# Performance work log

Hardware: AMD Instinct MI355X
Metric: run time of the kernel (lower is better)

## Reference

```python
import jax, jax.numpy as jnp
import numpy as np

D_IN = 768
D_H = 256
N_CTX = 4

def setup_inputs() -> dict:
    key = jax.random.key(0)
    ks = jax.random.split(key, 6)
    b, s = 64, 2048
    return {
        "last_hidden_states": jax.random.normal(ks[0], (b, s, D_IN), dtype=jnp.float32),
        "W1": jax.random.normal(ks[1], (D_IN, D_H), dtype=jnp.float32) / np.sqrt(D_IN),
        "b1": jnp.zeros((D_H,), dtype=jnp.float32),
        "context_vector": jax.random.normal(ks[2], (D_H, N_CTX), dtype=jnp.float32),
        "W2": jax.random.normal(ks[3], (N_CTX * D_IN, D_IN), dtype=jnp.float32) / np.sqrt(N_CTX * D_IN),
        "b2": jnp.zeros((D_IN,), dtype=jnp.float32),
    }

def reference(last_hidden_states, W1, b1, context_vector, W2, b2):
    b = last_hidden_states.shape[0]
    # h: [b, s, 256]
    h = jnp.tanh(jnp.einsum('bsd,dh->bsh', last_hidden_states, W1) + b1)
    # scores over sequence dim for each of 4 context vectors: [b, s, 4]
    scores = jax.nn.softmax(jnp.einsum('bsh,hc->bsc', h, context_vector), axis=1)
    # weighted sums: [b, 4, 768] -> flatten to [b, 3072]
    pooled = jnp.einsum('bsc,bsd->bcd', scores, last_hidden_states).reshape(b, -1)
    pooled = jax.nn.relu(pooled)
    return pooled @ W2 + b2
```

## Files before the change

kernel.cpp:

```cpp
#include <hip/hip_runtime.h>

typedef _Float16 f16x8 __attribute__((ext_vector_type(8)));
typedef _Float16 f16x4 __attribute__((ext_vector_type(4)));
typedef float f32x4 __attribute__((ext_vector_type(4)));

#define D_IN 768
#define D_H  256
#define SEQ  2048

__device__ __forceinline__ void gld16(const void* g, void* l) {
  __builtin_amdgcn_global_load_lds(
      (const __attribute__((address_space(1))) unsigned int*)g,
      (__attribute__((address_space(3))) unsigned int*)l, 16, 0, 0);
}

__global__ __launch_bounds__(256) void k0_w1t(const float* __restrict__ W1,
                                              _Float16* __restrict__ W1T) {
  __shared__ float tl[64][65];
  const int kb = blockIdx.x, nb = blockIdx.y, t = threadIdx.x;
#pragma unroll
  for (int rep = 0; rep < 16; ++rep) {
    const int row = rep * 4 + (t >> 6), col = t & 63;
    tl[row][col] = W1[(size_t)(kb * 64 + row) * D_H + nb * 64 + col];
  }
  __syncthreads();
#pragma unroll
  for (int rep = 0; rep < 16; ++rep) {
    const int n = rep * 4 + (t >> 6), k = t & 63;
    W1T[(size_t)(nb * 64 + n) * D_IN + kb * 64 + k] = (_Float16)tl[k][n];
  }
}

__global__ __launch_bounds__(256, 4) void kf_fused(const float* __restrict__ X,
    const _Float16* __restrict__ W1T, const float* __restrict__ b1,
    const float* __restrict__ C, _Float16* __restrict__ Ppart,
    float* __restrict__ stats) {
  __shared__ float    Al[64][32];
  __shared__ _Float16 Bl[256][32];
  __shared__ float    red2[2][64][4];
  __shared__ float    red[64][4];
  const int t = threadIdx.x;
  const int bid = blockIdx.x;
  const size_t M0 = (size_t)bid * 64;

  const int l = t & 63, w = t >> 6;
  const int ar0 = (w * 2 + 0) * 8 + (l >> 3);
  const int ar1 = (w * 2 + 1) * 8 + (l >> 3);
  const int aj = l & 7;
  const float* As0 = X + (M0 + ar0) * D_IN + ((aj ^ (ar0 & 7)) * 4);
  const float* As1 = X + (M0 + ar1) * D_IN + ((aj ^ (ar1 & 7)) * 4);
  char* Ad0 = (char*)Al + (w * 2 + 0) * 1024 + l * 16;
  char* Ad1 = (char*)Al + (w * 2 + 1) * 1024 + l * 16;
  const int bj = l & 3;
  const int bc0 = (w * 4 + 0) * 16 + (l >> 2);
  const int bc1 = (w * 4 + 1) * 16 + (l >> 2);
  const int bc2 = (w * 4 + 2) * 16 + (l >> 2);
  const int bc3 = (w * 4 + 3) * 16 + (l >> 2);
  const _Float16* Bs0 = W1T + (size_t)bc0 * D_IN + ((bj ^ (bc0 & 3)) * 8);
  const _Float16* Bs1 = W1T + (size_t)bc1 * D_IN + ((bj ^ (bc1 & 3)) * 8);
  const _Float16* Bs2 = W1T + (size_t)bc2 * D_IN + ((bj ^ (bc2 & 3)) * 8);
  const _Float16* Bs3 = W1T + (size_t)bc3 * D_IN + ((bj ^ (bc3 & 3)) * 8);
  char* Bd0 = (char*)Bl + (w * 4 + 0) * 1024 + l * 16;
  char* Bd1 = (char*)Bl + (w * 4 + 1) * 1024 + l * 16;
  char* Bd2 = (char*)Bl + (w * 4 + 2) * 1024 + l * 16;
  char* Bd3 = (char*)Bl + (w * 4 + 3) * 1024 + l * 16;

  const int wm = w >> 1, wn = w & 1;
  const int l15 = l & 15, kg = l >> 4;
  const int r0 = wm * 32 + l15, r1 = r0 + 16;
  const int sA0lo = ((2 * kg) ^ (r0 & 7)) * 4, sA0hi = ((2 * kg + 1) ^ (r0 & 7)) * 4;
  const int sA1lo = ((2 * kg) ^ (r1 & 7)) * 4, sA1hi = ((2 * kg + 1) ^ (r1 & 7)) * 4;

  f32x4 acc[2][8];
#pragma unroll
  for (int i = 0; i < 2; ++i)
#pragma unroll
    for (int n = 0; n < 8; ++n) acc[i][n] = f32x4{0.f, 0.f, 0.f, 0.f};

  for (int kt = 0; kt < 24; ++kt) {
    const int ko = kt * 32;
    gld16(As0 + ko, Ad0);
    gld16(As1 + ko, Ad1);
    gld16(Bs0 + ko, Bd0);
    gld16(Bs1 + ko, Bd1);
    gld16(Bs2 + ko, Bd2);
    gld16(Bs3 + ko, Bd3);
    __syncthreads();

    const float4 a0lo = *(const float4*)&Al[r0][sA0lo];
    const float4 a0hi = *(const float4*)&Al[r0][sA0hi];
    const float4 a1lo = *(const float4*)&Al[r1][sA1lo];
    const float4 a1hi = *(const float4*)&Al[r1][sA1hi];
    f16x8 af0, af1;
    af0[0] = (_Float16)a0lo.x; af0[1] = (_Float16)a0lo.y;
    af0[2] = (_Float16)a0lo.z; af0[3] = (_Float16)a0lo.w;
    af0[4] = (_Float16)a0hi.x; af0[5] = (_Float16)a0hi.y;
    af0[6] = (_Float16)a0hi.z; af0[7] = (_Float16)a0hi.w;
    af1[0] = (_Float16)a1lo.x; af1[1] = (_Float16)a1lo.y;
    af1[2] = (_Float16)a1lo.z; af1[3] = (_Float16)a1lo.w;
    af1[4] = (_Float16)a1hi.x; af1[5] = (_Float16)a1hi.y;
    af1[6] = (_Float16)a1hi.z; af1[7] = (_Float16)a1hi.w;
#pragma unroll
    for (int n = 0; n < 8; ++n) {
      const int col = wn * 128 + n * 16 + l15;
      const f16x8 bf = *(const f16x8*)&Bl[col][(kg ^ (col & 3)) * 8];
      acc[0][n] = __builtin_amdgcn_mfma_f32_16x16x32_f16(af0, bf, acc[0][n], 0, 0, 0);
      acc[1][n] = __builtin_amdgcn_mfma_f32_16x16x32_f16(af1, bf, acc[1][n], 0, 0, 0);
    }
    __syncthreads();
  }

  float part[2][4][4];
#pragma unroll
  for (int i = 0; i < 2; ++i)
#pragma unroll
    for (int r = 0; r < 4; ++r)
#pragma unroll
      for (int c = 0; c < 4; ++c) part[i][r][c] = 0.f;

#pragma unroll
  for (int n = 0; n < 8; ++n) {
    const int col = wn * 128 + n * 16 + l15;
    const float4 c4 = *(const float4*)(C + col * 4);
    const float bv = b1[col];
#pragma unroll
    for (int i = 0; i < 2; ++i)
#pragma unroll
      for (int r = 0; r < 4; ++r) {
        float z = acc[i][n][r] + bv;
        z = fminf(fmaxf(z, -15.f), 15.f);
        const float e = __expf(2.f * z);
        const float h = (e - 1.f) / (e + 1.f);
        part[i][r][0] += h * c4.x;
        part[i][r][1] += h * c4.y;
        part[i][r][2] += h * c4.z;
        part[i][r][3] += h * c4.w;
      }
  }
#pragma unroll
  for (int off = 1; off < 16; off <<= 1) {
#pragma unroll
    for (int i = 0; i < 2; ++i)
#pragma unroll
      for (int r = 0; r < 4; ++r)
#pragma unroll
        for (int c = 0; c < 4; ++c)
          part[i][r][c] += __shfl_xor(part[i][r][c], off, 64);
  }
  if (l15 == 0) {
#pragma unroll
    for (int i = 0; i < 2; ++i)
#pragma unroll
      for (int r = 0; r < 4; ++r)
#pragma unroll
        for (int c = 0; c < 4; ++c)
          red2[wn][wm * 32 + i * 16 + kg * 4 + r][c] = part[i][r][c];
  }
  __syncthreads();

  {
    const int r = t >> 2, c = t & 3;
    red[r][c] = red2[0][r][c] + red2[1][r][c];
  }
  __syncthreads();
  {
    const int c = t >> 6, r = t & 63;
    const float v = red[r][c];
    float m = v;
#pragma unroll
    for (int off = 1; off < 64; off <<= 1) m = fmaxf(m, __shfl_xor(m, off, 64));
    const float e = __expf(v - m);
    red[r][c] = e;
    float s = e;
#pragma unroll
    for (int off = 1; off < 64; off <<= 1) s += __shfl_xor(s, off, 64);
    if (r == 0) {
      stats[(size_t)bid * 8 + c * 2]     = m;
      stats[(size_t)bid * 8 + c * 2 + 1] = s;
    }
  }
  __syncthreads();

  if (t < 192) {
    float pacc[4][4];
#pragma unroll
    for (int c = 0; c < 4; ++c)
#pragma unroll
      for (int j = 0; j < 4; ++j) pacc[c][j] = 0.f;
    const float* Xp = X + M0 * D_IN + t * 4;
#pragma unroll 4
    for (int r = 0; r < 64; ++r) {
      const float4 x4 = *(const float4*)(Xp + (size_t)r * D_IN);
      const float4 w4 = *(const float4*)&red[r][0];
      const float wc[4] = {w4.x, w4.y, w4.z, w4.w};
      const float xv[4] = {x4.x, x4.y, x4.z, x4.w};
#pragma unroll
      for (int c = 0; c < 4; ++c)
#pragma unroll
        for (int j = 0; j < 4; ++j) pacc[c][j] += wc[c] * xv[j];
    }
#pragma unroll
    for (int c = 0; c < 4; ++c) {
      f16x4 o;
#pragma unroll
      for (int j = 0; j < 4; ++j) o[j] = (_Float16)pacc[c][j];
      *(f16x4*)&Ppart[(size_t)bid * 3072 + c * 768 + t * 4] = o;
    }
  }
}

__global__ __launch_bounds__(256) void kc_combine(const _Float16* __restrict__ Ppart,
    const float* __restrict__ stats, float* __restrict__ pooled) {
  const int b = blockIdx.x, t = threadIdx.x;
  __shared__ float sm[32][8];
  __shared__ float Mc[4], Dc[4], fw[32][4];
  sm[t >> 3][t & 7] = stats[((size_t)b * 32 + (t >> 3)) * 8 + (t & 7)];
  __syncthreads();
  if (t < 4) {
    float m = sm[0][t * 2];
#pragma unroll
    for (int blk = 1; blk < 32; ++blk) m = fmaxf(m, sm[blk][t * 2]);
    Mc[t] = m;
  }
  __syncthreads();
  if (t < 128) {
    const int blk = t >> 2, c = t & 3;
    fw[blk][c] = __expf(sm[blk][c * 2] - Mc[c]);
  }
  __syncthreads();
  if (t < 4) {
    float s = 0.f;
#pragma unroll
    for (int blk = 0; blk < 32; ++blk) s += fw[blk][t] * sm[blk][t * 2 + 1];
    Dc[t] = 1.f / s;
  }
  __syncthreads();
#pragma unroll
  for (int c = 0; c < 4; ++c) {
#pragma unroll
    for (int rep = 0; rep < 3; ++rep) {
      const int d = rep * 256 + t;
      float acc = 0.f;
#pragma unroll 4
      for (int blk = 0; blk < 32; ++blk)
        acc += fw[blk][c] * (float)Ppart[((size_t)(b * 32 + blk)) * 3072 + c * 768 + d];
      pooled[(size_t)b * 3072 + c * 768 + d] = fmaxf(acc * Dc[c], 0.f);
    }
  }
}

__global__ __launch_bounds__(256) void k4_partial(const float* __restrict__ pooled,
                                                  const float* __restrict__ W2,
                                                  float* __restrict__ partial) {
  const int jc = blockIdx.x, kc = blockIdx.y, t = threadIdx.x;
  __shared__ float plds[64 * 192];
  __shared__ float sum2[64][64];
  for (int idx = t; idx < 64 * 192; idx += 256) {
    const int b = idx / 192, k = idx - b * 192;
    plds[idx] = pooled[(size_t)b * 3072 + kc * 192 + k];
  }
  __syncthreads();
  const int j = t & 63, kp = t >> 6;
  float acc[64];
#pragma unroll
  for (int b = 0; b < 64; ++b) acc[b] = 0.f;
  const float* W2p = W2 + (size_t)(kc * 192 + kp * 48) * D_IN + jc * 64 + j;
  const float* pb = plds + kp * 48;
  for (int ki = 0; ki < 48; ki += 4) {
    const float w0 = W2p[(size_t)(ki + 0) * D_IN];
    const float w1 = W2p[(size_t)(ki + 1) * D_IN];
    const float w2 = W2p[(size_t)(ki + 2) * D_IN];
    const float w3 = W2p[(size_t)(ki + 3) * D_IN];
#pragma unroll
    for (int b = 0; b < 64; ++b) {
      const float4 p4 = *(const float4*)(pb + b * 192 + ki);
      acc[b] += p4.x * w0 + p4.y * w1 + p4.z * w2 + p4.w * w3;
    }
  }
#pragma unroll
  for (int p = 0; p < 4; ++p) {
    if (kp == p) {
      if (p == 0) {
#pragma unroll
        for (int b = 0; b < 64; ++b) sum2[b][j] = acc[b];
      } else {
#pragma unroll
        for (int b = 0; b < 64; ++b) sum2[b][j] += acc[b];
      }
    }
    __syncthreads();
  }
  for (int idx = t; idx < 4096; idx += 256) {
    const int b = idx >> 6, jj = idx & 63;
    partial[(size_t)kc * 49152 + (size_t)b * D_IN + jc * 64 + jj] = sum2[b][jj];
  }
}

__global__ __launch_bounds__(256) void k5_final(const float* __restrict__ partial,
                                                const float* __restrict__ b2,
                                                float* __restrict__ out) {
  const int o = blockIdx.x * 256 + threadIdx.x;
  float v = b2[o % D_IN];
#pragma unroll
  for (int p = 0; p < 16; ++p) v += partial[(size_t)p * 49152 + o];
  out[o] = v;
}

extern "C" void kernel_launch(void* const* d_in, const int* in_sizes, int n_in,
                              void* d_out, int out_size, void* d_ws, size_t ws_size,
                              hipStream_t stream) {
  const float* X  = (const float*)d_in[0];
  const float* W1 = (const float*)d_in[1];
  const float* b1 = (const float*)d_in[2];
  const float* C  = (const float*)d_in[3];
  const float* W2 = (const float*)d_in[4];
  const float* b2 = (const float*)d_in[5];
  float* out = (float*)d_out;
  char* ws = (char*)d_ws;
  _Float16* W1T   = (_Float16*)ws;
  float* pooled   = (float*)(ws + 393216);
  float* stats    = (float*)(ws + 1179648);
  _Float16* Ppart = (_Float16*)(ws + 1245184);
  float* partial  = (float*)(ws + 1245184);

  k0_w1t    <<<dim3(12, 4), 256, 0, stream>>>(W1, W1T);
  kf_fused  <<<2048,        256, 0, stream>>>(X, W1T, b1, C, Ppart, stats);
  kc_combine<<<64,          256, 0, stream>>>(Ppart, stats, pooled);
  k4_partial<<<dim3(12,16), 256, 0, stream>>>(pooled, W2, partial);
  k5_final  <<<192,         256, 0, stream>>>(partial, b2, out);
}
```

Before: 307.5 us.

## Double-buffer LDS tiles in fused GEMM to overlap global loads with MFMA

Splits the A and B LDS tiles into two buffers and restructures the K loop so the loads for tile k+2 are issued while tile k is computed, with explicit vmcnt waits and s_barriers. The goal is to hide global-to-LDS latency that the old single-buffer load-sync-compute loop exposed. In exchange the kernel uses twice the LDS, so launch bounds drop from 4 to 3 blocks per CU, which may reduce occupancy. The pooled-sum loop unroll is also raised from 4 to 8.

```diff
diff --git a/kernel.cpp b/kernel.cpp
--- a/kernel.cpp
+++ b/kernel.cpp
@@ -31,12 +31,12 @@
   }
 }
 
-__global__ __launch_bounds__(256, 4) void kf_fused(const float* __restrict__ X,
+__global__ __launch_bounds__(256, 3) void kf_fused(const float* __restrict__ X,
     const _Float16* __restrict__ W1T, const float* __restrict__ b1,
     const float* __restrict__ C, _Float16* __restrict__ Ppart,
     float* __restrict__ stats) {
-  __shared__ float    Al[64][32];
-  __shared__ _Float16 Bl[256][32];
+  __shared__ float    Al[2][64][32];
+  __shared__ _Float16 Bl[2][256][32];
   __shared__ float    red2[2][64][4];
   __shared__ float    red[64][4];
   const int t = threadIdx.x;
@@ -49,8 +49,8 @@
   const int aj = l & 7;
   const float* As0 = X + (M0 + ar0) * D_IN + ((aj ^ (ar0 & 7)) * 4);
   const float* As1 = X + (M0 + ar1) * D_IN + ((aj ^ (ar1 & 7)) * 4);
-  char* Ad0 = (char*)Al + (w * 2 + 0) * 1024 + l * 16;
-  char* Ad1 = (char*)Al + (w * 2 + 1) * 1024 + l * 16;
+  const int ad0 = (w * 2 + 0) * 1024 + l * 16;
+  const int ad1 = (w * 2 + 1) * 1024 + l * 16;
   const int bj = l & 3;
   const int bc0 = (w * 4 + 0) * 16 + (l >> 2);
   const int bc1 = (w * 4 + 1) * 16 + (l >> 2);
@@ -60,10 +60,10 @@
   const _Float16* Bs1 = W1T + (size_t)bc1 * D_IN + ((bj ^ (bc1 & 3)) * 8);
   const _Float16* Bs2 = W1T + (size_t)bc2 * D_IN + ((bj ^ (bc2 & 3)) * 8);
   const _Float16* Bs3 = W1T + (size_t)bc3 * D_IN + ((bj ^ (bc3 & 3)) * 8);
-  char* Bd0 = (char*)Bl + (w * 4 + 0) * 1024 + l * 16;
-  char* Bd1 = (char*)Bl + (w * 4 + 1) * 1024 + l * 16;
-  char* Bd2 = (char*)Bl + (w * 4 + 2) * 1024 + l * 16;
-  char* Bd3 = (char*)Bl + (w * 4 + 3) * 1024 + l * 16;
+  const int bd0 = (w * 4 + 0) * 1024 + l * 16;
+  const int bd1 = (w * 4 + 1) * 1024 + l * 16;
+  const int bd2 = (w * 4 + 2) * 1024 + l * 16;
+  const int bd3 = (w * 4 + 3) * 1024 + l * 16;
 
   const int wm = w >> 1, wn = w & 1;
   const int l15 = l & 15, kg = l >> 4;
@@ -77,20 +77,23 @@
 #pragma unroll
     for (int n = 0; n < 8; ++n) acc[i][n] = f32x4{0.f, 0.f, 0.f, 0.f};
 
-  for (int kt = 0; kt < 24; ++kt) {
+  auto issue6 = [&](int kt, int bsel) {
     const int ko = kt * 32;
-    gld16(As0 + ko, Ad0);
-    gld16(As1 + ko, Ad1);
-    gld16(Bs0 + ko, Bd0);
-    gld16(Bs1 + ko, Bd1);
-    gld16(Bs2 + ko, Bd2);
-    gld16(Bs3 + ko, Bd3);
-    __syncthreads();
-
-    const float4 a0lo = *(const float4*)&Al[r0][sA0lo];
-    const float4 a0hi = *(const float4*)&Al[r0][sA0hi];
-    const float4 a1lo = *(const float4*)&Al[r1][sA1lo];
-    const float4 a1hi = *(const float4*)&Al[r1][sA1hi];
+    char* ab = (char*)&Al[bsel][0][0];
+    char* bb = (char*)&Bl[bsel][0][0];
+    gld16(As0 + ko, ab + ad0);
+    gld16(As1 + ko, ab + ad1);
+    gld16(Bs0 + ko, bb + bd0);
+    gld16(Bs1 + ko, bb + bd1);
+    gld16(Bs2 + ko, bb + bd2);
+    gld16(Bs3 + ko, bb + bd3);
+  };
+
+  auto compute = [&](int bsel) {
+    const float4 a0lo = *(const float4*)&Al[bsel][r0][sA0lo];
+    const float4 a0hi = *(const float4*)&Al[bsel][r0][sA0hi];
+    const float4 a1lo = *(const float4*)&Al[bsel][r1][sA1lo];
+    const float4 a1hi = *(const float4*)&Al[bsel][r1][sA1hi];
     f16x8 af0, af1;
     af0[0] = (_Float16)a0lo.x; af0[1] = (_Float16)a0lo.y;
     af0[2] = (_Float16)a0lo.z; af0[3] = (_Float16)a0lo.w;
@@ -103,12 +106,39 @@
 #pragma unroll
     for (int n = 0; n < 8; ++n) {
       const int col = wn * 128 + n * 16 + l15;
-      const f16x8 bf = *(const f16x8*)&Bl[col][(kg ^ (col & 3)) * 8];
+      const f16x8 bf = *(const f16x8*)&Bl[bsel][col][(kg ^ (col & 3)) * 8];
       acc[0][n] = __builtin_amdgcn_mfma_f32_16x16x32_f16(af0, bf, acc[0][n], 0, 0, 0);
       acc[1][n] = __builtin_amdgcn_mfma_f32_16x16x32_f16(af1, bf, acc[1][n], 0, 0, 0);
     }
-    __syncthreads();
-  }
+  };
+
+  issue6(0, 0);
+  issue6(1, 1);
+
+  for (int kp = 0; kp < 11; ++kp) {
+#pragma unroll
+    for (int par = 0; par < 2; ++par) {
+      const int kt = 2 * kp + par;
+      asm volatile("s_waitcnt vmcnt(6)" ::: "memory");
+      __builtin_amdgcn_sched_barrier(0);
+      __builtin_amdgcn_s_barrier();
+      compute(par);
+      __builtin_amdgcn_sched_barrier(0);
+      __builtin_amdgcn_s_barrier();
+      if (kt < 22) issue6(kt + 2, par);
+      __builtin_amdgcn_sched_barrier(0);
+    }
+  }
+  asm volatile("s_waitcnt vmcnt(6)" ::: "memory");
+  __builtin_amdgcn_sched_barrier(0);
+  __builtin_amdgcn_s_barrier();
+  compute(0);
+  __builtin_amdgcn_sched_barrier(0);
+  __builtin_amdgcn_s_barrier();
+  asm volatile("s_waitcnt vmcnt(0)" ::: "memory");
+  __builtin_amdgcn_sched_barrier(0);
+  __builtin_amdgcn_s_barrier();
+  compute(1);
 
   float part[2][4][4];
 #pragma unroll
@@ -188,7 +218,7 @@
 #pragma unroll
       for (int j = 0; j < 4; ++j) pacc[c][j] = 0.f;
     const float* Xp = X + M0 * D_IN + t * 4;
-#pragma unroll 4
+#pragma unroll 8
     for (int r = 0; r < 64; ++r) {
       const float4 x4 = *(const float4*)(Xp + (size_t)r * D_IN);
       const float4 w4 = *(const float4*)&red[r][0];
```

Result: faster. 279.7 us (-9.0%).
